# Optimization experiments

Measured on AMD Instinct MI355X. Metric: run time of the kernel, lower is better.

Reference implementation:

```python
import jax, jax.numpy as jnp
import numpy as np

NUM_SEQS = 32
KV_LEN = 2048          # cached context length per sequence
NUM_HEADS = 16
HEAD_SIZE = 128
SCALE = 0.08838834764831845  # 1/sqrt(HEAD_SIZE)
TOTAL_SLOTS = NUM_SEQS * KV_LEN


def setup_inputs() -> dict:
    key = jax.random.key(0)
    kq, kk, kv, kc = jax.random.split(key, 4)
    q = jax.random.normal(kq, (NUM_SEQS, NUM_HEADS, HEAD_SIZE), dtype=jnp.float32)
    k = jax.random.normal(kk, (NUM_SEQS, NUM_HEADS, HEAD_SIZE), dtype=jnp.float32)
    v = jax.random.normal(kv, (NUM_SEQS, NUM_HEADS, HEAD_SIZE), dtype=jnp.float32)
    kv_cache = jax.random.normal(kc, (2, TOTAL_SLOTS, NUM_HEADS, HEAD_SIZE), dtype=jnp.float32)
    # each sequence owns slots [i*KV_LEN, (i+1)*KV_LEN); new token written at the last slot
    slot_mapping = jnp.arange(NUM_SEQS, dtype=jnp.int64) * KV_LEN + (KV_LEN - 1)
    return {"q": q, "k": k, "v": v, "kv_cache": kv_cache, "slot_mapping": slot_mapping}


def reference(q, k, v, kv_cache, slot_mapping):
    # 1) reshape_and_cache: scatter new k/v into the paged cache at slot_mapping
    kv_cache = kv_cache.at[0, slot_mapping].set(k)
    kv_cache = kv_cache.at[1, slot_mapping].set(v)
    # 2) paged attention decode: each query attends over its own contiguous slot range
    keys = kv_cache[0].reshape(NUM_SEQS, KV_LEN, NUM_HEADS, HEAD_SIZE)
    vals = kv_cache[1].reshape(NUM_SEQS, KV_LEN, NUM_HEADS, HEAD_SIZE)
    scores = jnp.einsum("shd,sthd->sht", q, keys) * SCALE  # [seqs, heads, kv_len]
    probs = jax.nn.softmax(scores, axis=-1)
    out = jnp.einsum("sht,sthd->shd", probs, vals)         # [seqs, heads, head_size]
    return out
```

## Files before the change

### kernel.cpp

```cpp
#include <hip/hip_runtime.h>

constexpr int NUM_SEQS  = 32;
constexpr int KV_LEN    = 2048;
constexpr int NUM_HEADS = 16;
constexpr int HEAD_SIZE = 128;
constexpr float SCALE   = 0.08838834764831845f;

constexpr int HSTRIDE = NUM_HEADS * HEAD_SIZE;
constexpr size_t KV_PLANE = (size_t)NUM_SEQS * KV_LEN * HSTRIDE;

__global__ __launch_bounds__(256, 4)
void paged_decode_kernel(const float* __restrict__ q,
                         const float* __restrict__ knew,
                         const float* __restrict__ vnew,
                         const float* __restrict__ kv,
                         const int*  __restrict__ slot_map,
                         float* __restrict__ out)
{
    const int bid  = blockIdx.x;
    const int s    = bid >> 4;
    const int h    = bid & (NUM_HEADS - 1);
    const int tid  = threadIdx.x;
    const int half = tid >> 5;
    const int lane = tid & 31;

    __shared__ float sc[KV_LEN];
    __shared__ float red[4];
    __shared__ float s_inv;
    __shared__ float part[8][HEAD_SIZE];

    const int qoff = (s * NUM_HEADS + h) * HEAD_SIZE;
    const float* kbase = kv + (size_t)s * KV_LEN * HSTRIDE + (size_t)h * HEAD_SIZE;
    const float* vbase = kbase + KV_PLANE;
    const int t_new = slot_map[s] - s * KV_LEN;

    const float4 qv = *reinterpret_cast<const float4*>(q + qoff + lane * 4);

    for (int base = 0; base < KV_LEN; base += 32) {
        const int t0 = base + half * 4;

        const float* p0 = (t0 + 0 == t_new) ? (knew + qoff) : (kbase + (size_t)(t0 + 0) * HSTRIDE);
        const float* p1 = (t0 + 1 == t_new) ? (knew + qoff) : (kbase + (size_t)(t0 + 1) * HSTRIDE);
        const float* p2 = (t0 + 2 == t_new) ? (knew + qoff) : (kbase + (size_t)(t0 + 2) * HSTRIDE);
        const float* p3 = (t0 + 3 == t_new) ? (knew + qoff) : (kbase + (size_t)(t0 + 3) * HSTRIDE);

        const float4 k0 = *reinterpret_cast<const float4*>(p0 + lane * 4);
        const float4 k1 = *reinterpret_cast<const float4*>(p1 + lane * 4);
        const float4 k2 = *reinterpret_cast<const float4*>(p2 + lane * 4);
        const float4 k3 = *reinterpret_cast<const float4*>(p3 + lane * 4);

        float d0 = fmaf(k0.x, qv.x, fmaf(k0.y, qv.y, fmaf(k0.z, qv.z, k0.w * qv.w)));
        float d1 = fmaf(k1.x, qv.x, fmaf(k1.y, qv.y, fmaf(k1.z, qv.z, k1.w * qv.w)));
        float d2 = fmaf(k2.x, qv.x, fmaf(k2.y, qv.y, fmaf(k2.z, qv.z, k2.w * qv.w)));
        float d3 = fmaf(k3.x, qv.x, fmaf(k3.y, qv.y, fmaf(k3.z, qv.z, k3.w * qv.w)));

        #pragma unroll
        for (int off = 16; off > 0; off >>= 1) {
            d0 += __shfl_xor(d0, off);
            d1 += __shfl_xor(d1, off);
            d2 += __shfl_xor(d2, off);
            d3 += __shfl_xor(d3, off);
        }
        if (lane == 0) {
            sc[t0 + 0] = d0 * SCALE;
            sc[t0 + 1] = d1 * SCALE;
            sc[t0 + 2] = d2 * SCALE;
            sc[t0 + 3] = d3 * SCALE;
        }
    }
    __syncthreads();

    float m = -1e30f;
    #pragma unroll
    for (int t = tid; t < KV_LEN; t += 256) m = fmaxf(m, sc[t]);
    #pragma unroll
    for (int off = 32; off > 0; off >>= 1) m = fmaxf(m, __shfl_xor(m, off));
    if ((tid & 63) == 0) red[tid >> 6] = m;
    __syncthreads();
    const float mblk = fmaxf(fmaxf(red[0], red[1]), fmaxf(red[2], red[3]));

    float lsum = 0.f;
    #pragma unroll
    for (int t = tid; t < KV_LEN; t += 256) {
        const float e = __expf(sc[t] - mblk);
        sc[t] = e;
        lsum += e;
    }
    #pragma unroll
    for (int off = 32; off > 0; off >>= 1) lsum += __shfl_xor(lsum, off);
    __syncthreads();
    if ((tid & 63) == 0) red[tid >> 6] = lsum;
    __syncthreads();
    if (tid == 0) s_inv = 1.0f / (red[0] + red[1] + red[2] + red[3]);
    __syncthreads();
    const float inv = s_inv;

    float4 acc = make_float4(0.f, 0.f, 0.f, 0.f);
    for (int base = 0; base < KV_LEN; base += 32) {
        const int t0 = base + half * 4;

        const float* p0 = (t0 + 0 == t_new) ? (vnew + qoff) : (vbase + (size_t)(t0 + 0) * HSTRIDE);
        const float* p1 = (t0 + 1 == t_new) ? (vnew + qoff) : (vbase + (size_t)(t0 + 1) * HSTRIDE);
        const float* p2 = (t0 + 2 == t_new) ? (vnew + qoff) : (vbase + (size_t)(t0 + 2) * HSTRIDE);
        const float* p3 = (t0 + 3 == t_new) ? (vnew + qoff) : (vbase + (size_t)(t0 + 3) * HSTRIDE);

        const float4 v0 = *reinterpret_cast<const float4*>(p0 + lane * 4);
        const float4 v1 = *reinterpret_cast<const float4*>(p1 + lane * 4);
        const float4 v2 = *reinterpret_cast<const float4*>(p2 + lane * 4);
        const float4 v3 = *reinterpret_cast<const float4*>(p3 + lane * 4);

        const float w0 = sc[t0 + 0];
        const float w1 = sc[t0 + 1];
        const float w2 = sc[t0 + 2];
        const float w3 = sc[t0 + 3];

        acc.x = fmaf(w0, v0.x, acc.x); acc.y = fmaf(w0, v0.y, acc.y);
        acc.z = fmaf(w0, v0.z, acc.z); acc.w = fmaf(w0, v0.w, acc.w);
        acc.x = fmaf(w1, v1.x, acc.x); acc.y = fmaf(w1, v1.y, acc.y);
        acc.z = fmaf(w1, v1.z, acc.z); acc.w = fmaf(w1, v1.w, acc.w);
        acc.x = fmaf(w2, v2.x, acc.x); acc.y = fmaf(w2, v2.y, acc.y);
        acc.z = fmaf(w2, v2.z, acc.z); acc.w = fmaf(w2, v2.w, acc.w);
        acc.x = fmaf(w3, v3.x, acc.x); acc.y = fmaf(w3, v3.y, acc.y);
        acc.z = fmaf(w3, v3.z, acc.z); acc.w = fmaf(w3, v3.w, acc.w);
    }

    *reinterpret_cast<float4*>(&part[half][lane * 4]) = acc;
    __syncthreads();

    if (tid < HEAD_SIZE) {
        float o = 0.f;
        #pragma unroll
        for (int i = 0; i < 8; ++i) o += part[i][tid];
        out[qoff + tid] = o * inv;
    }
}

extern "C" void kernel_launch(void* const* d_in, const int* in_sizes, int n_in,
                              void* d_out, int out_size, void* d_ws, size_t ws_size,
                              hipStream_t stream) {
    const float* q    = (const float*)d_in[0];
    const float* k    = (const float*)d_in[1];
    const float* v    = (const float*)d_in[2];
    const float* kv   = (const float*)d_in[3];
    const int*   slot = (const int*)d_in[4];
    float* out = (float*)d_out;

    dim3 grid(NUM_SEQS * NUM_HEADS);
    dim3 block(256);
    hipLaunchKernelGGL(paged_decode_kernel, grid, block, 0, stream,
                       q, k, v, kv, slot, out);
}
```

Measured before the change: 1.281 ms.

## Split KV sequence across blocks with flash-decoding partials and combine kernel

Splits each (sequence, head) KV range into 8 partitions, so 4096 blocks run instead of 512. Each block computes a local max, sum and unnormalized output into workspace, and a second kernel rescales and combines them. It also widens each warp-group's load batch from 4 to 8 rows to raise memory-level parallelism. The cost is a second launch and a small workspace round-trip, in exchange for filling the GPU on a bandwidth-bound decode.

```diff
diff --git a/kernel.cpp b/kernel.cpp
--- a/kernel.cpp
+++ b/kernel.cpp
@@ -9,119 +9,114 @@
 constexpr int HSTRIDE = NUM_HEADS * HEAD_SIZE;
 constexpr size_t KV_PLANE = (size_t)NUM_SEQS * KV_LEN * HSTRIDE;
 
+constexpr int NPART = 8;
+constexpr int PART  = KV_LEN / NPART;
+
 __global__ __launch_bounds__(256, 4)
-void paged_decode_kernel(const float* __restrict__ q,
-                         const float* __restrict__ knew,
-                         const float* __restrict__ vnew,
-                         const float* __restrict__ kv,
-                         const int*  __restrict__ slot_map,
-                         float* __restrict__ out)
+void decode_partial(const float* __restrict__ q,
+                    const float* __restrict__ knew,
+                    const float* __restrict__ vnew,
+                    const float* __restrict__ kv,
+                    const int*  __restrict__ slot_map,
+                    float* __restrict__ acc_ws,
+                    float* __restrict__ ml_ws)
 {
     const int bid  = blockIdx.x;
-    const int s    = bid >> 4;
-    const int h    = bid & (NUM_HEADS - 1);
+    const int p    = bid & (NPART - 1);
+    const int h    = (bid >> 3) & (NUM_HEADS - 1);
+    const int s    = bid >> 7;
     const int tid  = threadIdx.x;
     const int half = tid >> 5;
     const int lane = tid & 31;
 
-    __shared__ float sc[KV_LEN];
+    __shared__ float sc[PART];
     __shared__ float red[4];
-    __shared__ float s_inv;
     __shared__ float part[8][HEAD_SIZE];
 
     const int qoff = (s * NUM_HEADS + h) * HEAD_SIZE;
     const float* kbase = kv + (size_t)s * KV_LEN * HSTRIDE + (size_t)h * HEAD_SIZE;
     const float* vbase = kbase + KV_PLANE;
     const int t_new = slot_map[s] - s * KV_LEN;
+    const int tbase = p * PART;
 
     const float4 qv = *reinterpret_cast<const float4*>(q + qoff + lane * 4);
 
-    for (int base = 0; base < KV_LEN; base += 32) {
-        const int t0 = base + half * 4;
+    #pragma unroll 1
+    for (int it = 0; it < 4; ++it) {
+        const int t0 = tbase + it * 64 + half * 8;
 
-        const float* p0 = (t0 + 0 == t_new) ? (knew + qoff) : (kbase + (size_t)(t0 + 0) * HSTRIDE);
-        const float* p1 = (t0 + 1 == t_new) ? (knew + qoff) : (kbase + (size_t)(t0 + 1) * HSTRIDE);
-        const float* p2 = (t0 + 2 == t_new) ? (knew + qoff) : (kbase + (size_t)(t0 + 2) * HSTRIDE);
-        const float* p3 = (t0 + 3 == t_new) ? (knew + qoff) : (kbase + (size_t)(t0 + 3) * HSTRIDE);
+        const float* pp[8];
+        #pragma unroll
+        for (int j = 0; j < 8; ++j) {
+            const int t = t0 + j;
+            pp[j] = (t == t_new) ? (knew + qoff) : (kbase + (size_t)t * HSTRIDE);
+        }
+        float4 kk[8];
+        #pragma unroll
+        for (int j = 0; j < 8; ++j)
+            kk[j] = *reinterpret_cast<const float4*>(pp[j] + lane * 4);
 
-        const float4 k0 = *reinterpret_cast<const float4*>(p0 + lane * 4);
-        const float4 k1 = *reinterpret_cast<const float4*>(p1 + lane * 4);
-        const float4 k2 = *reinterpret_cast<const float4*>(p2 + lane * 4);
-        const float4 k3 = *reinterpret_cast<const float4*>(p3 + lane * 4);
-
-        float d0 = fmaf(k0.x, qv.x, fmaf(k0.y, qv.y, fmaf(k0.z, qv.z, k0.w * qv.w)));
-        float d1 = fmaf(k1.x, qv.x, fmaf(k1.y, qv.y, fmaf(k1.z, qv.z, k1.w * qv.w)));
-        float d2 = fmaf(k2.x, qv.x, fmaf(k2.y, qv.y, fmaf(k2.z, qv.z, k2.w * qv.w)));
-        float d3 = fmaf(k3.x, qv.x, fmaf(k3.y, qv.y, fmaf(k3.z, qv.z, k3.w * qv.w)));
+        float d[8];
+        #pragma unroll
+        for (int j = 0; j < 8; ++j)
+            d[j] = fmaf(kk[j].x, qv.x, fmaf(kk[j].y, qv.y,
+                   fmaf(kk[j].z, qv.z, kk[j].w * qv.w)));
 
         #pragma unroll
         for (int off = 16; off > 0; off >>= 1) {
-            d0 += __shfl_xor(d0, off);
-            d1 += __shfl_xor(d1, off);
-            d2 += __shfl_xor(d2, off);
-            d3 += __shfl_xor(d3, off);
+            #pragma unroll
+            for (int j = 0; j < 8; ++j) d[j] += __shfl_xor(d[j], off);
         }
         if (lane == 0) {
-            sc[t0 + 0] = d0 * SCALE;
-            sc[t0 + 1] = d1 * SCALE;
-            sc[t0 + 2] = d2 * SCALE;
-            sc[t0 + 3] = d3 * SCALE;
+            const int o = it * 64 + half * 8;
+            #pragma unroll
+            for (int j = 0; j < 8; ++j) sc[o + j] = d[j] * SCALE;
         }
     }
     __syncthreads();
 
-    float m = -1e30f;
-    #pragma unroll
-    for (int t = tid; t < KV_LEN; t += 256) m = fmaxf(m, sc[t]);
+    float m = sc[tid];
     #pragma unroll
     for (int off = 32; off > 0; off >>= 1) m = fmaxf(m, __shfl_xor(m, off));
     if ((tid & 63) == 0) red[tid >> 6] = m;
     __syncthreads();
-    const float mblk = fmaxf(fmaxf(red[0], red[1]), fmaxf(red[2], red[3]));
+    m = fmaxf(fmaxf(red[0], red[1]), fmaxf(red[2], red[3]));
 
-    float lsum = 0.f;
+    const float e = __expf(sc[tid] - m);
+    float l = e;
     #pragma unroll
-    for (int t = tid; t < KV_LEN; t += 256) {
-        const float e = __expf(sc[t] - mblk);
-        sc[t] = e;
-        lsum += e;
-    }
-    #pragma unroll
-    for (int off = 32; off > 0; off >>= 1) lsum += __shfl_xor(lsum, off);
+    for (int off = 32; off > 0; off >>= 1) l += __shfl_xor(l, off);
     __syncthreads();
-    if ((tid & 63) == 0) red[tid >> 6] = lsum;
+    sc[tid] = e;
+    if ((tid & 63) == 0) red[tid >> 6] = l;
     __syncthreads();
-    if (tid == 0) s_inv = 1.0f / (red[0] + red[1] + red[2] + red[3]);
-    __syncthreads();
-    const float inv = s_inv;
+    l = red[0] + red[1] + red[2] + red[3];
 
     float4 acc = make_float4(0.f, 0.f, 0.f, 0.f);
-    for (int base = 0; base < KV_LEN; base += 32) {
-        const int t0 = base + half * 4;
+    #pragma unroll 1
+    for (int it = 0; it < 4; ++it) {
+        const int t0 = tbase + it * 64 + half * 8;
 
-        const float* p0 = (t0 + 0 == t_new) ? (vnew + qoff) : (vbase + (size_t)(t0 + 0) * HSTRIDE);
-        const float* p1 = (t0 + 1 == t_new) ? (vnew + qoff) : (vbase + (size_t)(t0 + 1) * HSTRIDE);
-        const float* p2 = (t0 + 2 == t_new) ? (vnew + qoff) : (vbase + (size_t)(t0 + 2) * HSTRIDE);
-        const float* p3 = (t0 + 3 == t_new) ? (vnew + qoff) : (vbase + (size_t)(t0 + 3) * HSTRIDE);
+        const float* pp[8];
+        #pragma unroll
+        for (int j = 0; j < 8; ++j) {
+            const int t = t0 + j;
+            pp[j] = (t == t_new) ? (vnew + qoff) : (vbase + (size_t)t * HSTRIDE);
+        }
+        float4 vv[8];
+        #pragma unroll
+        for (int j = 0; j < 8; ++j)
+            vv[j] = *reinterpret_cast<const float4*>(pp[j] + lane * 4);
 
-        const float4 v0 = *reinterpret_cast<const float4*>(p0 + lane * 4);
-        const float4 v1 = *reinterpret_cast<const float4*>(p1 + lane * 4);
-        const float4 v2 = *reinterpret_cast<const float4*>(p2 + lane * 4);
-        const float4 v3 = *reinterpret_cast<const float4*>(p3 + lane * 4);
-
-        const float w0 = sc[t0 + 0];
-        const float w1 = sc[t0 + 1];
-        const float w2 = sc[t0 + 2];
-        const float w3 = sc[t0 + 3];
-
-        acc.x = fmaf(w0, v0.x, acc.x); acc.y = fmaf(w0, v0.y, acc.y);
-        acc.z = fmaf(w0, v0.z, acc.z); acc.w = fmaf(w0, v0.w, acc.w);
-        acc.x = fmaf(w1, v1.x, acc.x); acc.y = fmaf(w1, v1.y, acc.y);
-        acc.z = fmaf(w1, v1.z, acc.z); acc.w = fmaf(w1, v1.w, acc.w);
-        acc.x = fmaf(w2, v2.x, acc.x); acc.y = fmaf(w2, v2.y, acc.y);
-        acc.z = fmaf(w2, v2.z, acc.z); acc.w = fmaf(w2, v2.w, acc.w);
-        acc.x = fmaf(w3, v3.x, acc.x); acc.y = fmaf(w3, v3.y, acc.y);
-        acc.z = fmaf(w3, v3.z, acc.z); acc.w = fmaf(w3, v3.w, acc.w);
+        const int o = it * 64 + half * 8;
+        #pragma unroll
+        for (int j = 0; j < 8; ++j) {
+            const float w = sc[o + j];
+            acc.x = fmaf(w, vv[j].x, acc.x);
+            acc.y = fmaf(w, vv[j].y, acc.y);
+            acc.z = fmaf(w, vv[j].z, acc.z);
+            acc.w = fmaf(w, vv[j].w, acc.w);
+        }
     }
 
     *reinterpret_cast<float4*>(&part[half][lane * 4]) = acc;
@@ -131,8 +126,37 @@
         float o = 0.f;
         #pragma unroll
         for (int i = 0; i < 8; ++i) o += part[i][tid];
-        out[qoff + tid] = o * inv;
+        acc_ws[(size_t)bid * HEAD_SIZE + tid] = o;
     }
+    if (tid == 0) {
+        ml_ws[bid * 2 + 0] = m;
+        ml_ws[bid * 2 + 1] = l;
+    }
+}
+
+__global__ __launch_bounds__(128)
+void decode_combine(const float* __restrict__ acc_ws,
+                    const float* __restrict__ ml_ws,
+                    float* __restrict__ out)
+{
+    const int sh = blockIdx.x;
+    const int d  = threadIdx.x;
+
+    float M = -1e30f;
+    #pragma unroll
+    for (int p = 0; p < NPART; ++p)
+        M = fmaxf(M, ml_ws[(sh * NPART + p) * 2]);
+
+    float L = 0.f, o = 0.f;
+    #pragma unroll
+    for (int p = 0; p < NPART; ++p) {
+        const float mp = ml_ws[(sh * NPART + p) * 2 + 0];
+        const float lp = ml_ws[(sh * NPART + p) * 2 + 1];
+        const float w  = __expf(mp - M);
+        L += w * lp;
+        o = fmaf(w, acc_ws[(size_t)(sh * NPART + p) * HEAD_SIZE + d], o);
+    }
+    out[sh * HEAD_SIZE + d] = o / L;
 }
 
 extern "C" void kernel_launch(void* const* d_in, const int* in_sizes, int n_in,
@@ -145,8 +169,12 @@
     const int*   slot = (const int*)d_in[4];
     float* out = (float*)d_out;
 
-    dim3 grid(NUM_SEQS * NUM_HEADS);
-    dim3 block(256);
-    hipLaunchKernelGGL(paged_decode_kernel, grid, block, 0, stream,
-                       q, k, v, kv, slot, out);
+    constexpr int NBLK = NUM_SEQS * NUM_HEADS * NPART;
+    float* acc_ws = (float*)d_ws;
+    float* ml_ws  = acc_ws + (size_t)NBLK * HEAD_SIZE;
+
+    hipLaunchKernelGGL(decode_partial, dim3(NBLK), dim3(256), 0, stream,
+                       q, k, v, kv, slot, acc_ws, ml_ws);
+    hipLaunchKernelGGL(decode_combine, dim3(NUM_SEQS * NUM_HEADS), dim3(128), 0, stream,
+                       acc_ws, ml_ws, out);
 }
```

Measured after the change: 1.324 ms. +3.4%, slower.
